# Performance work log

Measured on AMD Instinct MI355X. Metric: run time of the kernel, lower is better.

## Reference

```python
import jax, jax.numpy as jnp
import numpy as np

B, H, S, D = 2, 16, 2048, 64  # batch, heads, seq (q_len=k_len), head dim (d_k=d_v)


def setup_inputs() -> dict:
    key = jax.random.key(0)
    kq, kk, kv = jax.random.split(key, 3)
    Q = jax.random.normal(kq, (B, H, S, D), dtype=jnp.float32)
    K = jax.random.normal(kk, (B, H, S, D), dtype=jnp.float32)
    V = jax.random.normal(kv, (B, H, S, D), dtype=jnp.float32)
    # causal 0/1 mask [q_len, k_len]; zeros get filled with -inf like masked_fill_
    mask = jnp.tril(jnp.ones((S, S), dtype=jnp.int32))
    return {"Q": Q, "K": K, "V": V, "mask": mask}


def reference(Q, K, V, mask):
    scale = K.shape[-1] ** 0.5
    # [B,H,q,k] = Q @ K^T / sqrt(d_k)
    scores = jnp.einsum("bhqd,bhkd->bhqk", Q, K) / scale
    # mask broadcast over batch/heads; mask==0 -> -inf
    scores = jnp.where(mask == 0, jnp.float32(-jnp.inf), scores)
    attn = jax.nn.softmax(scores, axis=-1)
    return jnp.einsum("bhqk,bhkd->bhqd", attn, V)
```

## Files before the change

### kernel.cpp

```cpp
#include <hip/hip_runtime.h>

#define S_LEN 2048
#define DHEAD 64
#define BK 64
#define NBH 32
#define QSCALE 0.18033688011112042f
#define LTHR 1.125899907e15f
#define LSCL 8.881784197e-16f

typedef float f32x4 __attribute__((ext_vector_type(4)));
typedef __bf16 bf16x8 __attribute__((ext_vector_type(8)));
typedef unsigned short u16x8 __attribute__((ext_vector_type(8)));
typedef unsigned short u16x4 __attribute__((ext_vector_type(4)));
typedef unsigned int   u32x4 __attribute__((ext_vector_type(4)));
typedef unsigned int   u32x2 __attribute__((ext_vector_type(2)));

static __device__ __forceinline__ unsigned short bfr(float f) {
    return __builtin_bit_cast(unsigned short, (__bf16)f);
}
static __device__ __forceinline__ int swz(int row, int cb) {
    return row * 128 + (cb ^ ((row & 7) << 4));
}

#if __has_builtin(__builtin_amdgcn_permlane32_swap) && __has_builtin(__builtin_amdgcn_permlane16_swap)
static __device__ __forceinline__ void plswap32(unsigned& a, unsigned& b) {
    u32x2 r = __builtin_amdgcn_permlane32_swap(a, b, false, false);
    a = r[0]; b = r[1];
}
static __device__ __forceinline__ void plswap16(unsigned& a, unsigned& b) {
    u32x2 r = __builtin_amdgcn_permlane16_swap(a, b, false, false);
    a = r[0]; b = r[1];
}
#else
static __device__ __forceinline__ void plswap32(unsigned& a, unsigned& b) {
    asm("v_permlane32_swap_b32 %0, %1" : "+v"(a), "+v"(b));
}
static __device__ __forceinline__ void plswap16(unsigned& a, unsigned& b) {
    asm("v_permlane16_swap_b32 %0, %1" : "+v"(a), "+v"(b));
}
#endif

__global__ __launch_bounds__(256)
void prep(const float* __restrict__ K, const float* __restrict__ V,
          unsigned short* __restrict__ Kb, unsigned short* __restrict__ Vt, int n4) {
    __shared__ unsigned short t2[64][72];
    if ((int)blockIdx.x < 2048) {
        const int stride = 2048 * 256;
        for (int i = (int)blockIdx.x * 256 + threadIdx.x; i < n4; i += stride) {
            f32x4 v = ((const f32x4*)K)[i];
            u16x4 t;
            t[0] = bfr(v[0]); t[1] = bfr(v[1]); t[2] = bfr(v[2]); t[3] = bfr(v[3]);
            ((u16x4*)Kb)[i] = t;
        }
    } else {
        const int bid = (int)blockIdx.x - 2048;
        const int bh = bid >> 5;
        const int st = bid & 31;
        const int t  = threadIdx.x;
        {
            const int sl = t >> 2, d0 = (t & 3) * 16;
            const float* src = V + ((size_t)bh * S_LEN + st * 64 + sl) * DHEAD + d0;
#pragma unroll
            for (int j = 0; j < 4; ++j) {
                f32x4 v = *(const f32x4*)(src + j * 4);
#pragma unroll
                for (int e = 0; e < 4; ++e) t2[sl][d0 + j * 4 + e] = bfr(v[e]);
            }
        }
        __syncthreads();
        const int d = t >> 2, sc = (t & 3) * 16;
        u16x8 a, b;
#pragma unroll
        for (int r = 0; r < 8; ++r) { a[r] = t2[sc + r][d]; b[r] = t2[sc + 8 + r][d]; }
        unsigned short* dst = Vt + ((size_t)bh * DHEAD + d) * S_LEN + st * 64 + sc;
        *(u16x8*)dst = a;
        *(u16x8*)(dst + 8) = b;
    }
}

__global__ __launch_bounds__(256, 3)
void attn_pipe(const float* __restrict__ Qg,
               const unsigned short* __restrict__ Kb,
               const unsigned short* __restrict__ Vt,
               float* __restrict__ Og) {
    __shared__ __align__(16) unsigned short sK[2][BK * DHEAD];
    __shared__ __align__(16) unsigned short sV[2][DHEAD * BK];

    const int tid  = threadIdx.x;
    const int lane = tid & 63;
    const int w    = tid >> 6;
    const int idx = (int)blockIdx.x >> 5;
    const int bh  = (int)blockIdx.x & (NBH - 1);
    const int jj  = idx & 7, k4 = idx >> 3;
    const int blk_q = (k4 == 0) ? 31 - jj : (k4 == 1) ? jj
                    : (k4 == 2) ? 16 + jj : 15 - jj;
    const int q0 = blk_q * 64;
    const size_t base = (size_t)bh * (S_LEN * DHEAD);

    const int c = lane & 15;
    const int h = lane >> 4;

    const int srow = w * 8 + (lane >> 3);
    const int ch8  = ((lane & 7) ^ (lane >> 3)) * 8;
    const unsigned short* pK = Kb + base + (size_t)srow * DHEAD + ch8;
    const unsigned short* pV = Vt + base + (size_t)srow * S_LEN + ch8;

    auto issue = [&](int buf, int kt) {
        unsigned short* dK = &sK[buf][w * 512];
        unsigned short* dV = &sV[buf][w * 512];
        const unsigned short* gk = pK + (size_t)kt * 4096;
        const unsigned short* gv = pV + kt * 64;
#pragma unroll
        for (int i = 0; i < 2; ++i) {
            __builtin_amdgcn_global_load_lds(
                (const __attribute__((address_space(1))) unsigned int*)(gk + i * 2048),
                (__attribute__((address_space(3))) unsigned int*)(dK + i * 2048),
                16, 0, 0);
            __builtin_amdgcn_global_load_lds(
                (const __attribute__((address_space(1))) unsigned int*)(gv + (size_t)i * 32 * S_LEN),
                (__attribute__((address_space(3))) unsigned int*)(dV + i * 2048),
                16, 0, 0);
        }
    };

    bf16x8 qf[2];
    {
        const int qrow = q0 + w * 16 + c;
        const float* qp = Qg + base + (size_t)qrow * DHEAD + h * 8;
#pragma unroll
        for (int kk = 0; kk < 2; ++kk) {
            f32x4 a = *(const f32x4*)(qp + kk * 32);
            f32x4 b = *(const f32x4*)(qp + kk * 32 + 4);
            u16x8 t;
#pragma unroll
            for (int j = 0; j < 4; ++j) {
                t[j]     = bfr(a[j] * QSCALE);
                t[4 + j] = bfr(b[j] * QSCALE);
            }
            qf[kk] = __builtin_bit_cast(bf16x8, t);
        }
    }

    bf16x8 onesf;
    {
        u16x8 t;
#pragma unroll
        for (int j = 0; j < 8; ++j) t[j] = 0x3F80;
        onesf = __builtin_bit_cast(bf16x8, t);
    }

    int offAB[4][2];
#pragma unroll
    for (int n = 0; n < 4; ++n)
#pragma unroll
        for (int kk = 0; kk < 2; ++kk)
            offAB[n][kk] = swz(n * 16 + c, (kk * 32 + h * 8) * 2);

    f32x4 o[4];
#pragma unroll
    for (int dn = 0; dn < 4; ++dn) o[dn] = (f32x4){0.f, 0.f, 0.f, 0.f};
    f32x4 l4 = (f32x4){0.f, 0.f, 0.f, 0.f};
    float m_run = 0.f;
    const int qg = q0 + w * 16 + c;

    issue(0, 0);
    __syncthreads();
    if (blk_q >= 1) issue(1, 1);

    f32x4 st[4];
    {
        const char* sKc = (const char*)&sK[0][0];
#pragma unroll
        for (int n = 0; n < 4; ++n) {
            f32x4 acc = (f32x4){0.f, 0.f, 0.f, 0.f};
#pragma unroll
            for (int kk = 0; kk < 2; ++kk) {
                u16x8 kf = *(const u16x8*)(sKc + offAB[n][kk]);
                acc = __builtin_amdgcn_mfma_f32_16x16x32_bf16(
                        __builtin_bit_cast(bf16x8, kf), qf[kk], acc, 0, 0, 0);
            }
            st[n] = acc;
        }
    }
    bf16x8 vf[4][2];
    {
        const char* sVc = (const char*)&sV[0][0];
#pragma unroll
        for (int dn = 0; dn < 4; ++dn)
#pragma unroll
            for (int kk = 0; kk < 2; ++kk)
                vf[dn][kk] = __builtin_bit_cast(bf16x8,
                                *(const u16x8*)(sVc + offAB[dn][kk]));
    }

    for (int i = 0; i <= blk_q; ++i) {
        f32x4 st2[4];
        if (i < blk_q) {
            __syncthreads();
            if (i + 2 <= blk_q) issue(i & 1, i + 2);

            const char* sKc = (const char*)&sK[(i + 1) & 1][0];
            const float mb = -m_run;
#pragma unroll
            for (int n = 0; n < 4; ++n) {
                f32x4 acc = (f32x4){mb, mb, mb, mb};
#pragma unroll
                for (int kk = 0; kk < 2; ++kk) {
                    u16x8 kf = *(const u16x8*)(sKc + offAB[n][kk]);
                    acc = __builtin_amdgcn_mfma_f32_16x16x32_bf16(
                            __builtin_bit_cast(bf16x8, kf), qf[kk], acc, 0, 0, 0);
                }
                st2[n] = acc;
            }
        }

        if (i == blk_q) {
#pragma unroll
            for (int n = 0; n < 4; ++n)
#pragma unroll
                for (int r = 0; r < 4; ++r)
                    if (i * BK + n * 16 + 4 * h + r > qg) st[n][r] = -INFINITY;
        }

#pragma unroll
        for (int n = 0; n < 4; ++n)
#pragma unroll
            for (int r = 0; r < 4; ++r)
                st[n][r] = exp2f(st[n][r]);

        unsigned pd[4][2];
#pragma unroll
        for (int n = 0; n < 4; ++n) {
            pd[n][0] = (unsigned)bfr(st[n][0]) | ((unsigned)bfr(st[n][1]) << 16);
            pd[n][1] = (unsigned)bfr(st[n][2]) | ((unsigned)bfr(st[n][3]) << 16);
        }
        bf16x8 pb[2];
#pragma unroll
        for (int kk = 0; kk < 2; ++kk) {
            u32x4 fr;
#pragma unroll
            for (int X = 0; X < 2; ++X) {
                unsigned u = pd[2 * kk][X], v = pd[2 * kk + 1][X];
                plswap32(u, v);
                plswap16(u, v);
                fr[X]     = u;
                fr[2 + X] = v;
            }
            pb[kk] = __builtin_bit_cast(bf16x8, fr);
        }

        __builtin_amdgcn_s_setprio(1);
#pragma unroll
        for (int kk = 0; kk < 2; ++kk) {
            l4 = __builtin_amdgcn_mfma_f32_16x16x32_bf16(onesf, pb[kk], l4, 0, 0, 0);
#pragma unroll
            for (int dn = 0; dn < 4; ++dn)
                o[dn] = __builtin_amdgcn_mfma_f32_16x16x32_bf16(
                          vf[dn][kk], pb[kk], o[dn], 0, 0, 0);
        }
        __builtin_amdgcn_s_setprio(0);

        if (i < blk_q) {
            const char* sVc = (const char*)&sV[(i + 1) & 1][0];
#pragma unroll
            for (int dn = 0; dn < 4; ++dn)
#pragma unroll
                for (int kk = 0; kk < 2; ++kk)
                    vf[dn][kk] = __builtin_bit_cast(bf16x8,
                                    *(const u16x8*)(sVc + offAB[dn][kk]));
        }

        if (__builtin_expect(l4[0] > LTHR, 0)) {
            m_run += 50.0f;
            l4 *= LSCL;
#pragma unroll
            for (int dn = 0; dn < 4; ++dn) o[dn] *= LSCL;
            if (i < blk_q) {
#pragma unroll
                for (int n = 0; n < 4; ++n)
#pragma unroll
                    for (int r = 0; r < 4; ++r) st2[n][r] -= 50.0f;
            }
        }

        if (i < blk_q) {
#pragma unroll
            for (int n = 0; n < 4; ++n) st[n] = st2[n];
        }
    }

    const float inv = 1.0f / l4[0];
    float* op = Og + base + (size_t)qg * DHEAD + h * 4;
#pragma unroll
    for (int dn = 0; dn < 4; ++dn) {
        f32x4 t = o[dn] * inv;
        *(f32x4*)(op + dn * 16) = t;
    }
}

__global__ __launch_bounds__(256)
void attn_fb(const float* __restrict__ Qg, const float* __restrict__ K32,
             const float* __restrict__ V32, float* __restrict__ Og) {
    __shared__ __align__(16) unsigned short sK[2][BK * DHEAD];
    __shared__ __align__(16) unsigned short sV[2][DHEAD * BK];
    __shared__ __align__(16) unsigned short sP[4][16 * BK];

    const int tid  = threadIdx.x;
    const int lane = tid & 63;
    const int w    = tid >> 6;
    const int blk_q = 31 - ((int)blockIdx.x >> 5);
    const int bh    = (int)blockIdx.x & (NBH - 1);
    const int q0    = blk_q * 64;
    const size_t base = (size_t)bh * (S_LEN * DHEAD);

    const int col = lane & 15;
    const int hi  = lane >> 4;
    const int vkb = (tid >> 4) * 4;
    const int vdb = (tid & 15) * 4;
    const int fkr = tid >> 2;
    const int fkc = (tid & 3) * 16;

    f32x4 kr32[4], vr32[4];
    auto stage_issue = [&](int kt) {
        const float* kp = K32 + base + (size_t)(kt * BK + fkr) * DHEAD + fkc;
#pragma unroll
        for (int j = 0; j < 4; ++j) kr32[j] = *(const f32x4*)(kp + j * 4);
        const float* vp = V32 + base + (size_t)(kt * BK + vkb) * DHEAD + vdb;
#pragma unroll
        for (int j = 0; j < 4; ++j) vr32[j] = *(const f32x4*)(vp + j * DHEAD);
    };
    auto stage_write = [&](int buf) {
        char* sKb_ = (char*)&sK[buf][0];
        char* sVb_ = (char*)&sV[buf][0];
        u16x8 p0, p1;
#pragma unroll
        for (int j = 0; j < 4; ++j) {
            p0[j] = bfr(kr32[0][j]); p0[4 + j] = bfr(kr32[1][j]);
            p1[j] = bfr(kr32[2][j]); p1[4 + j] = bfr(kr32[3][j]);
        }
        *(u16x8*)(sKb_ + swz(fkr, fkc * 2))      = p0;
        *(u16x8*)(sKb_ + swz(fkr, fkc * 2 + 16)) = p1;
#pragma unroll
        for (int dd = 0; dd < 4; ++dd) {
            u16x4 t;
#pragma unroll
            for (int j = 0; j < 4; ++j) t[j] = bfr(vr32[j][dd]);
            *(u16x4*)(sVb_ + swz(vdb + dd, vkb * 2)) = t;
        }
    };

    bf16x8 qf[2];
    {
        const int qrow = q0 + w * 16 + col;
        const float* qp = Qg + base + (size_t)qrow * DHEAD + hi * 8;
#pragma unroll
        for (int kk = 0; kk < 2; ++kk) {
            f32x4 a = *(const f32x4*)(qp + kk * 32);
            f32x4 b = *(const f32x4*)(qp + kk * 32 + 4);
            u16x8 t;
#pragma unroll
            for (int j = 0; j < 4; ++j) {
                t[j]     = bfr(a[j] * QSCALE);
                t[4 + j] = bfr(b[j] * QSCALE);
            }
            qf[kk] = __builtin_bit_cast(bf16x8, t);
        }
    }

    int offAB[4][2];
#pragma unroll
    for (int n = 0; n < 4; ++n)
#pragma unroll
        for (int kk = 0; kk < 2; ++kk)
            offAB[n][kk] = swz(n * 16 + col, (kk * 32 + hi * 8) * 2);
    char* sPw = (char*)&sP[w][0];
    int offPS[4], offPL[2];
#pragma unroll
    for (int n = 0; n < 4; ++n)
        offPS[n] = col * 128 + ((n * 32 + hi * 8) ^ ((col & 7) << 4));
#pragma unroll
    for (int kk = 0; kk < 2; ++kk)
        offPL[kk] = col * 128 + ((kk * 64 + hi * 16) ^ ((col & 7) << 4));

    f32x4 o[4];
#pragma unroll
    for (int dn = 0; dn < 4; ++dn) o[dn] = (f32x4){0.f, 0.f, 0.f, 0.f};
    float m_run = -INFINITY, l_run = 0.f;

    stage_issue(0);
    stage_write(0);
    __syncthreads();

    int cur = 0;
    for (int kt = 0; kt <= blk_q; ++kt) {
        const char* sKc = (const char*)&sK[cur][0];
        const char* sVc = (const char*)&sV[cur][0];
        if (kt < blk_q) stage_issue(kt + 1);

        f32x4 st[4];
#pragma unroll
        for (int n = 0; n < 4; ++n) {
            f32x4 acc = (f32x4){0.f, 0.f, 0.f, 0.f};
#pragma unroll
            for (int kk = 0; kk < 2; ++kk) {
                u16x8 kf = *(const u16x8*)(sKc + offAB[n][kk]);
                acc = __builtin_amdgcn_mfma_f32_16x16x32_bf16(
                        __builtin_bit_cast(bf16x8, kf), qf[kk], acc, 0, 0, 0);
            }
            st[n] = acc;
        }
        if (kt == blk_q) {
            const int qg = q0 + w * 16 + col;
#pragma unroll
            for (int n = 0; n < 4; ++n)
#pragma unroll
                for (int r = 0; r < 4; ++r)
                    if (kt * BK + n * 16 + hi * 4 + r > qg) st[n][r] = -INFINITY;
        }
        float mx = fmaxf(fmaxf(st[0][0], st[0][1]), fmaxf(st[0][2], st[0][3]));
#pragma unroll
        for (int n = 1; n < 4; ++n)
            mx = fmaxf(mx, fmaxf(fmaxf(st[n][0], st[n][1]), fmaxf(st[n][2], st[n][3])));
        mx = fmaxf(mx, __shfl_xor(mx, 16));
        mx = fmaxf(mx, __shfl_xor(mx, 32));
        if (!__all(mx <= m_run + 8.0f)) {
            const float mn = fmaxf(m_run, mx);
            const float al = exp2f(m_run - mn);
            m_run = mn;
            l_run *= al;
#pragma unroll
            for (int dn = 0; dn < 4; ++dn) o[dn] *= al;
        }
        float sum = 0.f;
#pragma unroll
        for (int n = 0; n < 4; ++n)
#pragma unroll
            for (int r = 0; r < 4; ++r) {
                float p = exp2f(st[n][r] - m_run);
                st[n][r] = p;
                sum += p;
            }
        sum += __shfl_xor(sum, 16);
        sum += __shfl_xor(sum, 32);
        l_run += sum;
#pragma unroll
        for (int n = 0; n < 4; ++n) {
            u16x4 t;
#pragma unroll
            for (int r = 0; r < 4; ++r) t[r] = bfr(st[n][r]);
            *(u16x4*)(sPw + offPS[n]) = t;
        }
        bf16x8 pb[2];
#pragma unroll
        for (int kk = 0; kk < 2; ++kk)
            pb[kk] = __builtin_bit_cast(bf16x8, *(const u16x8*)(sPw + offPL[kk]));
#pragma unroll
        for (int dn = 0; dn < 4; ++dn)
#pragma unroll
            for (int kk = 0; kk < 2; ++kk) {
                u16x8 vfr = *(const u16x8*)(sVc + offAB[dn][kk]);
                o[dn] = __builtin_amdgcn_mfma_f32_16x16x32_bf16(
                          __builtin_bit_cast(bf16x8, vfr), pb[kk], o[dn], 0, 0, 0);
            }
        if (kt < blk_q) stage_write(cur ^ 1);
        __syncthreads();
        cur ^= 1;
    }

    const float inv = 1.0f / l_run;
    const int qg = q0 + w * 16 + col;
    float* op = Og + base + (size_t)qg * DHEAD + hi * 4;
#pragma unroll
    for (int dn = 0; dn < 4; ++dn) {
        f32x4 t = o[dn] * inv;
        *(f32x4*)(op + dn * 16) = t;
    }
}

extern "C" void kernel_launch(void* const* d_in, const int* in_sizes, int n_in,
                              void* d_out, int out_size, void* d_ws, size_t ws_size,
                              hipStream_t stream) {
    const float* Q = (const float*)d_in[0];
    const float* K = (const float*)d_in[1];
    const float* V = (const float*)d_in[2];
    float* O = (float*)d_out;

    const size_t nelem   = (size_t)NBH * S_LEN * DHEAD;
    const size_t kvBytes = 2 * nelem * sizeof(unsigned short);

    if (ws_size >= kvBytes) {
        unsigned short* Kb = (unsigned short*)d_ws;
        unsigned short* Vt = Kb + nelem;
        prep<<<3072, 256, 0, stream>>>(K, V, Kb, Vt, (int)(nelem / 4));
        attn_pipe<<<dim3(32 * NBH), 256, 0, stream>>>(Q, Kb, Vt, O);
    } else {
        attn_fb<<<dim3(32 * NBH), 256, 0, stream>>>(Q, K, V, O);
    }
}
```

Baseline: 54.05 us.

## Replace LDS double-buffered K/V pipeline with direct global-to-register loads

The attention kernel no longer stages K and V tiles through shared memory with async global-to-LDS loads and barriers. Each wave now loads its K and V fragments straight from global memory into registers, relying on L2/L1 for reuse across the four waves of a block. It also drops the software pipelining that computed the next tile's scores early, and replaces the load-balanced query-block ordering with a simple descending order. This removes barrier and LDS traffic but multiplies global/L1 reads by the wave count and exposes load latency without explicit prefetch.

```diff
diff --git a/kernel.cpp b/kernel.cpp
--- a/kernel.cpp
+++ b/kernel.cpp
@@ -79,54 +79,25 @@
 }
 
 __global__ __launch_bounds__(256, 3)
-void attn_pipe(const float* __restrict__ Qg,
-               const unsigned short* __restrict__ Kb,
-               const unsigned short* __restrict__ Vt,
-               float* __restrict__ Og) {
-    __shared__ __align__(16) unsigned short sK[2][BK * DHEAD];
-    __shared__ __align__(16) unsigned short sV[2][DHEAD * BK];
-
+void attn_nb(const float* __restrict__ Qg,
+             const unsigned short* __restrict__ Kb,
+             const unsigned short* __restrict__ Vt,
+             float* __restrict__ Og) {
     const int tid  = threadIdx.x;
     const int lane = tid & 63;
     const int w    = tid >> 6;
-    const int idx = (int)blockIdx.x >> 5;
-    const int bh  = (int)blockIdx.x & (NBH - 1);
-    const int jj  = idx & 7, k4 = idx >> 3;
-    const int blk_q = (k4 == 0) ? 31 - jj : (k4 == 1) ? jj
-                    : (k4 == 2) ? 16 + jj : 15 - jj;
-    const int q0 = blk_q * 64;
+    const int bh   = (int)blockIdx.x & (NBH - 1);
+    const int qb   = 31 - ((int)blockIdx.x >> 5);
+    const int q0   = qb * 64;
     const size_t base = (size_t)bh * (S_LEN * DHEAD);
 
     const int c = lane & 15;
     const int h = lane >> 4;
-
-    const int srow = w * 8 + (lane >> 3);
-    const int ch8  = ((lane & 7) ^ (lane >> 3)) * 8;
-    const unsigned short* pK = Kb + base + (size_t)srow * DHEAD + ch8;
-    const unsigned short* pV = Vt + base + (size_t)srow * S_LEN + ch8;
-
-    auto issue = [&](int buf, int kt) {
-        unsigned short* dK = &sK[buf][w * 512];
-        unsigned short* dV = &sV[buf][w * 512];
-        const unsigned short* gk = pK + (size_t)kt * 4096;
-        const unsigned short* gv = pV + kt * 64;
-#pragma unroll
-        for (int i = 0; i < 2; ++i) {
-            __builtin_amdgcn_global_load_lds(
-                (const __attribute__((address_space(1))) unsigned int*)(gk + i * 2048),
-                (__attribute__((address_space(3))) unsigned int*)(dK + i * 2048),
-                16, 0, 0);
-            __builtin_amdgcn_global_load_lds(
-                (const __attribute__((address_space(1))) unsigned int*)(gv + (size_t)i * 32 * S_LEN),
-                (__attribute__((address_space(3))) unsigned int*)(dV + i * 2048),
-                16, 0, 0);
-        }
-    };
+    const int qg = q0 + w * 16 + c;
 
     bf16x8 qf[2];
     {
-        const int qrow = q0 + w * 16 + c;
-        const float* qp = Qg + base + (size_t)qrow * DHEAD + h * 8;
+        const float* qp = Qg + base + (size_t)qg * DHEAD + h * 8;
 #pragma unroll
         for (int kk = 0; kk < 2; ++kk) {
             f32x4 a = *(const f32x4*)(qp + kk * 32);
@@ -149,77 +120,53 @@
         onesf = __builtin_bit_cast(bf16x8, t);
     }
 
-    int offAB[4][2];
-#pragma unroll
-    for (int n = 0; n < 4; ++n)
-#pragma unroll
-        for (int kk = 0; kk < 2; ++kk)
-            offAB[n][kk] = swz(n * 16 + c, (kk * 32 + h * 8) * 2);
+    const unsigned short* pK = Kb + base + (size_t)c * 64 + h * 8;
+    const unsigned short* pV = Vt + base + (size_t)c * S_LEN + h * 8;
 
     f32x4 o[4];
 #pragma unroll
     for (int dn = 0; dn < 4; ++dn) o[dn] = (f32x4){0.f, 0.f, 0.f, 0.f};
     f32x4 l4 = (f32x4){0.f, 0.f, 0.f, 0.f};
     float m_run = 0.f;
-    const int qg = q0 + w * 16 + c;
-
-    issue(0, 0);
-    __syncthreads();
-    if (blk_q >= 1) issue(1, 1);
-
-    f32x4 st[4];
-    {
-        const char* sKc = (const char*)&sK[0][0];
+
+    for (int kt = 0; kt <= qb; ++kt) {
+        const unsigned short* pKt = pK + kt * (BK * DHEAD);
+        const unsigned short* pVt = pV + kt * BK;
+
+        u16x8 kr[4][2];
+#pragma unroll
+        for (int n = 0; n < 4; ++n)
+#pragma unroll
+            for (int kk = 0; kk < 2; ++kk)
+                kr[n][kk] = *(const u16x8*)(pKt + n * (16 * DHEAD) + kk * 32);
+
+        const float mb = -m_run;
+        f32x4 st[4];
+        __builtin_amdgcn_s_setprio(1);
 #pragma unroll
         for (int n = 0; n < 4; ++n) {
-            f32x4 acc = (f32x4){0.f, 0.f, 0.f, 0.f};
-#pragma unroll
-            for (int kk = 0; kk < 2; ++kk) {
-                u16x8 kf = *(const u16x8*)(sKc + offAB[n][kk]);
+            f32x4 acc = (f32x4){mb, mb, mb, mb};
+#pragma unroll
+            for (int kk = 0; kk < 2; ++kk)
                 acc = __builtin_amdgcn_mfma_f32_16x16x32_bf16(
-                        __builtin_bit_cast(bf16x8, kf), qf[kk], acc, 0, 0, 0);
-            }
+                        __builtin_bit_cast(bf16x8, kr[n][kk]), qf[kk], acc, 0, 0, 0);
             st[n] = acc;
         }
-    }
-    bf16x8 vf[4][2];
-    {
-        const char* sVc = (const char*)&sV[0][0];
+        __builtin_amdgcn_s_setprio(0);
+
+        u16x8 vr[4][2];
 #pragma unroll
         for (int dn = 0; dn < 4; ++dn)
 #pragma unroll
             for (int kk = 0; kk < 2; ++kk)
-                vf[dn][kk] = __builtin_bit_cast(bf16x8,
-                                *(const u16x8*)(sVc + offAB[dn][kk]));
-    }
-
-    for (int i = 0; i <= blk_q; ++i) {
-        f32x4 st2[4];
-        if (i < blk_q) {
-            __syncthreads();
-            if (i + 2 <= blk_q) issue(i & 1, i + 2);
-
-            const char* sKc = (const char*)&sK[(i + 1) & 1][0];
-            const float mb = -m_run;
-#pragma unroll
-            for (int n = 0; n < 4; ++n) {
-                f32x4 acc = (f32x4){mb, mb, mb, mb};
-#pragma unroll
-                for (int kk = 0; kk < 2; ++kk) {
-                    u16x8 kf = *(const u16x8*)(sKc + offAB[n][kk]);
-                    acc = __builtin_amdgcn_mfma_f32_16x16x32_bf16(
-                            __builtin_bit_cast(bf16x8, kf), qf[kk], acc, 0, 0, 0);
-                }
-                st2[n] = acc;
-            }
-        }
-
-        if (i == blk_q) {
+                vr[dn][kk] = *(const u16x8*)(pVt + dn * (16 * S_LEN) + kk * 32);
+
+        if (kt == qb) {
 #pragma unroll
             for (int n = 0; n < 4; ++n)
 #pragma unroll
                 for (int r = 0; r < 4; ++r)
-                    if (i * BK + n * 16 + 4 * h + r > qg) st[n][r] = -INFINITY;
+                    if (kt * BK + n * 16 + 4 * h + r > qg) st[n][r] = -INFINITY;
         }
 
 #pragma unroll
@@ -256,36 +203,15 @@
 #pragma unroll
             for (int dn = 0; dn < 4; ++dn)
                 o[dn] = __builtin_amdgcn_mfma_f32_16x16x32_bf16(
-                          vf[dn][kk], pb[kk], o[dn], 0, 0, 0);
+                          __builtin_bit_cast(bf16x8, vr[dn][kk]), pb[kk], o[dn], 0, 0, 0);
         }
         __builtin_amdgcn_s_setprio(0);
-
-        if (i < blk_q) {
-            const char* sVc = (const char*)&sV[(i + 1) & 1][0];
-#pragma unroll
-            for (int dn = 0; dn < 4; ++dn)
-#pragma unroll
-                for (int kk = 0; kk < 2; ++kk)
-                    vf[dn][kk] = __builtin_bit_cast(bf16x8,
-                                    *(const u16x8*)(sVc + offAB[dn][kk]));
-        }
 
         if (__builtin_expect(l4[0] > LTHR, 0)) {
             m_run += 50.0f;
             l4 *= LSCL;
 #pragma unroll
             for (int dn = 0; dn < 4; ++dn) o[dn] *= LSCL;
-            if (i < blk_q) {
-#pragma unroll
-                for (int n = 0; n < 4; ++n)
-#pragma unroll
-                    for (int r = 0; r < 4; ++r) st2[n][r] -= 50.0f;
-            }
-        }
-
-        if (i < blk_q) {
-#pragma unroll
-            for (int n = 0; n < 4; ++n) st[n] = st2[n];
         }
     }
 
@@ -492,7 +418,7 @@
         unsigned short* Kb = (unsigned short*)d_ws;
         unsigned short* Vt = Kb + nelem;
         prep<<<3072, 256, 0, stream>>>(K, V, Kb, Vt, (int)(nelem / 4));
-        attn_pipe<<<dim3(32 * NBH), 256, 0, stream>>>(Q, Kb, Vt, O);
+        attn_nb<<<dim3(32 * NBH), 256, 0, stream>>>(Q, Kb, Vt, O);
     } else {
         attn_fb<<<dim3(32 * NBH), 256, 0, stream>>>(Q, K, V, O);
     }
```

After: 157.9 us. 2.92x slower.

## Split key dimension across warps with LDS reduction instead of per-warp query rows

Applied to the files above, without the earlier changes.

The attention kernel now gives each warp a 16-key slice of every 64-key tile across all 64 query rows, rather than 16 query rows across all keys. P stays in the MFMA output layout and feeds 16x16x16 MFMAs directly, which removes the permlane swaps and the running-max rescale check. Partial O and row sums from the four warps are combined through LDS at the end. The cost is more accumulator registers (occupancy hint lowered from 3 to 2), an end-of-kernel reduction, and no max subtraction, so exp2 overflow safety depends on the input score range.

```diff
diff --git a/kernel.cpp b/kernel.cpp
--- a/kernel.cpp
+++ b/kernel.cpp
@@ -5,15 +5,13 @@
 #define BK 64
 #define NBH 32
 #define QSCALE 0.18033688011112042f
-#define LTHR 1.125899907e15f
-#define LSCL 8.881784197e-16f
 
 typedef float f32x4 __attribute__((ext_vector_type(4)));
 typedef __bf16 bf16x8 __attribute__((ext_vector_type(8)));
+typedef __bf16 bf16x4 __attribute__((ext_vector_type(4)));
+typedef short  s16x4  __attribute__((ext_vector_type(4)));
 typedef unsigned short u16x8 __attribute__((ext_vector_type(8)));
 typedef unsigned short u16x4 __attribute__((ext_vector_type(4)));
-typedef unsigned int   u32x4 __attribute__((ext_vector_type(4)));
-typedef unsigned int   u32x2 __attribute__((ext_vector_type(2)));
 
 static __device__ __forceinline__ unsigned short bfr(float f) {
     return __builtin_bit_cast(unsigned short, (__bf16)f);
@@ -22,23 +20,19 @@
     return row * 128 + (cb ^ ((row & 7) << 4));
 }
 
-#if __has_builtin(__builtin_amdgcn_permlane32_swap) && __has_builtin(__builtin_amdgcn_permlane16_swap)
-static __device__ __forceinline__ void plswap32(unsigned& a, unsigned& b) {
-    u32x2 r = __builtin_amdgcn_permlane32_swap(a, b, false, false);
-    a = r[0]; b = r[1];
-}
-static __device__ __forceinline__ void plswap16(unsigned& a, unsigned& b) {
-    u32x2 r = __builtin_amdgcn_permlane16_swap(a, b, false, false);
-    a = r[0]; b = r[1];
-}
+static __device__ __forceinline__ f32x4 mfma16(bf16x4 a, bf16x4 b, f32x4 c) {
+#if __has_builtin(__builtin_amdgcn_mfma_f32_16x16x16_bf16)
+    return __builtin_amdgcn_mfma_f32_16x16x16_bf16(a, b, c, 0, 0, 0);
+#elif __has_builtin(__builtin_amdgcn_mfma_f32_16x16x16bf16_1k)
+    return __builtin_amdgcn_mfma_f32_16x16x16bf16_1k(
+        __builtin_bit_cast(s16x4, a), __builtin_bit_cast(s16x4, b), c, 0, 0, 0);
 #else
-static __device__ __forceinline__ void plswap32(unsigned& a, unsigned& b) {
-    asm("v_permlane32_swap_b32 %0, %1" : "+v"(a), "+v"(b));
-}
-static __device__ __forceinline__ void plswap16(unsigned& a, unsigned& b) {
-    asm("v_permlane16_swap_b32 %0, %1" : "+v"(a), "+v"(b));
-}
+    f32x4 d;
+    asm volatile("v_mfma_f32_16x16x16_bf16 %0, %1, %2, %3"
+                 : "=&v"(d) : "v"(a), "v"(b), "v"(c));
+    return d;
 #endif
+}
 
 __global__ __launch_bounds__(256)
 void prep(const float* __restrict__ K, const float* __restrict__ V,
@@ -78,13 +72,12 @@
     }
 }
 
-__global__ __launch_bounds__(256, 3)
-void attn_pipe(const float* __restrict__ Qg,
-               const unsigned short* __restrict__ Kb,
-               const unsigned short* __restrict__ Vt,
-               float* __restrict__ Og) {
-    __shared__ __align__(16) unsigned short sK[2][BK * DHEAD];
-    __shared__ __align__(16) unsigned short sV[2][DHEAD * BK];
+__global__ __launch_bounds__(256, 2)
+void attn_ks(const float* __restrict__ Qg,
+             const unsigned short* __restrict__ Kb,
+             const unsigned short* __restrict__ Vt,
+             float* __restrict__ Og) {
+    __shared__ __align__(16) char smem[35328];
 
     const int tid  = threadIdx.x;
     const int lane = tid & 63;
@@ -92,9 +85,9 @@
     const int idx = (int)blockIdx.x >> 5;
     const int bh  = (int)blockIdx.x & (NBH - 1);
     const int jj  = idx & 7, k4 = idx >> 3;
-    const int blk_q = (k4 == 0) ? 31 - jj : (k4 == 1) ? jj
-                    : (k4 == 2) ? 16 + jj : 15 - jj;
-    const int q0 = blk_q * 64;
+    const int qb  = (k4 == 0) ? 31 - jj : (k4 == 1) ? jj
+                  : (k4 == 2) ? 16 + jj : 15 - jj;
+    const int q0  = qb * 64;
     const size_t base = (size_t)bh * (S_LEN * DHEAD);
 
     const int c = lane & 15;
@@ -106,8 +99,8 @@
     const unsigned short* pV = Vt + base + (size_t)srow * S_LEN + ch8;
 
     auto issue = [&](int buf, int kt) {
-        unsigned short* dK = &sK[buf][w * 512];
-        unsigned short* dV = &sV[buf][w * 512];
+        unsigned short* dK = (unsigned short*)(smem + buf * 16384) + w * 512;
+        unsigned short* dV = (unsigned short*)(smem + buf * 16384 + 8192) + w * 512;
         const unsigned short* gk = pK + (size_t)kt * 4096;
         const unsigned short* gv = pV + kt * 64;
 #pragma unroll
@@ -123,9 +116,10 @@
         }
     };
 
-    bf16x8 qf[2];
-    {
-        const int qrow = q0 + w * 16 + c;
+    bf16x8 qf[4][2];
+#pragma unroll
+    for (int qg = 0; qg < 4; ++qg) {
+        const int qrow = q0 + qg * 16 + c;
         const float* qp = Qg + base + (size_t)qrow * DHEAD + h * 8;
 #pragma unroll
         for (int kk = 0; kk < 2; ++kk) {
@@ -137,164 +131,176 @@
                 t[j]     = bfr(a[j] * QSCALE);
                 t[4 + j] = bfr(b[j] * QSCALE);
             }
-            qf[kk] = __builtin_bit_cast(bf16x8, t);
-        }
-    }
-
-    bf16x8 onesf;
+            qf[qg][kk] = __builtin_bit_cast(bf16x8, t);
+        }
+    }
+
+    bf16x4 ones4;
     {
-        u16x8 t;
-#pragma unroll
-        for (int j = 0; j < 8; ++j) t[j] = 0x3F80;
-        onesf = __builtin_bit_cast(bf16x8, t);
-    }
-
-    int offAB[4][2];
-#pragma unroll
-    for (int n = 0; n < 4; ++n)
-#pragma unroll
-        for (int kk = 0; kk < 2; ++kk)
-            offAB[n][kk] = swz(n * 16 + c, (kk * 32 + h * 8) * 2);
-
-    f32x4 o[4];
-#pragma unroll
-    for (int dn = 0; dn < 4; ++dn) o[dn] = (f32x4){0.f, 0.f, 0.f, 0.f};
-    f32x4 l4 = (f32x4){0.f, 0.f, 0.f, 0.f};
-    float m_run = 0.f;
-    const int qg = q0 + w * 16 + c;
+        u16x4 t;
+#pragma unroll
+        for (int j = 0; j < 4; ++j) t[j] = 0x3F80;
+        ones4 = __builtin_bit_cast(bf16x4, t);
+    }
+
+    int offKA[2], offV[4];
+#pragma unroll
+    for (int kk = 0; kk < 2; ++kk)
+        offKA[kk] = swz(16 * w + c, (kk * 32 + h * 8) * 2);
+#pragma unroll
+    for (int dg = 0; dg < 4; ++dg)
+        offV[dg] = swz(dg * 16 + c, (16 * w + 4 * h) * 2);
+
+    int thr[4];
+#pragma unroll
+    for (int qg = 0; qg < 4; ++qg)
+        thr[qg] = qg * 16 + c - 16 * w - 4 * h;
+
+    f32x4 o[4][4];
+#pragma unroll
+    for (int dg = 0; dg < 4; ++dg)
+#pragma unroll
+        for (int qg = 0; qg < 4; ++qg) o[dg][qg] = (f32x4){0.f, 0.f, 0.f, 0.f};
+    f32x4 l4[4];
+#pragma unroll
+    for (int qg = 0; qg < 4; ++qg) l4[qg] = (f32x4){0.f, 0.f, 0.f, 0.f};
 
     issue(0, 0);
     __syncthreads();
-    if (blk_q >= 1) issue(1, 1);
+    if (qb >= 1) issue(1, 1);
 
     f32x4 st[4];
     {
-        const char* sKc = (const char*)&sK[0][0];
-#pragma unroll
-        for (int n = 0; n < 4; ++n) {
+        const char* Kc = smem;
+        bf16x8 kr0 = __builtin_bit_cast(bf16x8, *(const u16x8*)(Kc + offKA[0]));
+        bf16x8 kr1 = __builtin_bit_cast(bf16x8, *(const u16x8*)(Kc + offKA[1]));
+#pragma unroll
+        for (int qg = 0; qg < 4; ++qg) {
             f32x4 acc = (f32x4){0.f, 0.f, 0.f, 0.f};
-#pragma unroll
-            for (int kk = 0; kk < 2; ++kk) {
-                u16x8 kf = *(const u16x8*)(sKc + offAB[n][kk]);
-                acc = __builtin_amdgcn_mfma_f32_16x16x32_bf16(
-                        __builtin_bit_cast(bf16x8, kf), qf[kk], acc, 0, 0, 0);
-            }
-            st[n] = acc;
-        }
-    }
-    bf16x8 vf[4][2];
+            acc = __builtin_amdgcn_mfma_f32_16x16x32_bf16(kr0, qf[qg][0], acc, 0, 0, 0);
+            acc = __builtin_amdgcn_mfma_f32_16x16x32_bf16(kr1, qf[qg][1], acc, 0, 0, 0);
+            st[qg] = acc;
+        }
+        if (qb == 0) {
+#pragma unroll
+            for (int qg = 0; qg < 4; ++qg)
+#pragma unroll
+                for (int r = 0; r < 4; ++r)
+                    if (r > thr[qg]) st[qg][r] = -INFINITY;
+        }
+    }
+
+    for (int i = 0; i <= qb; ++i) {
+        const char* Vc = smem + (i & 1) * 16384 + 8192;
+        bf16x4 vf[4];
+#pragma unroll
+        for (int dg = 0; dg < 4; ++dg)
+            vf[dg] = __builtin_bit_cast(bf16x4, *(const u16x4*)(Vc + offV[dg]));
+
+        f32x4 st2[4];
+        if (i < qb) {
+            __syncthreads();
+            if (i + 2 <= qb) issue(i & 1, i + 2);
+
+            const char* Kc = smem + ((i + 1) & 1) * 16384;
+            bf16x8 kr0 = __builtin_bit_cast(bf16x8, *(const u16x8*)(Kc + offKA[0]));
+            bf16x8 kr1 = __builtin_bit_cast(bf16x8, *(const u16x8*)(Kc + offKA[1]));
+            __builtin_amdgcn_s_setprio(1);
+#pragma unroll
+            for (int qg = 0; qg < 4; ++qg) {
+                f32x4 acc = (f32x4){0.f, 0.f, 0.f, 0.f};
+                acc = __builtin_amdgcn_mfma_f32_16x16x32_bf16(kr0, qf[qg][0], acc, 0, 0, 0);
+                acc = __builtin_amdgcn_mfma_f32_16x16x32_bf16(kr1, qf[qg][1], acc, 0, 0, 0);
+                st2[qg] = acc;
+            }
+            __builtin_amdgcn_s_setprio(0);
+            if (i + 1 == qb) {
+#pragma unroll
+                for (int qg = 0; qg < 4; ++qg)
+#pragma unroll
+                    for (int r = 0; r < 4; ++r)
+                        if (r > thr[qg]) st2[qg][r] = -INFINITY;
+            }
+        }
+
+        bf16x4 pb[4];
+#pragma unroll
+        for (int qg = 0; qg < 4; ++qg) {
+            u16x4 t;
+#pragma unroll
+            for (int r = 0; r < 4; ++r)
+                t[r] = bfr(exp2f(st[qg][r]));
+            pb[qg] = __builtin_bit_cast(bf16x4, t);
+        }
+
+        __builtin_amdgcn_s_setprio(1);
+#pragma unroll
+        for (int qg = 0; qg < 4; ++qg)
+            l4[qg] = mfma16(ones4, pb[qg], l4[qg]);
+#pragma unroll
+        for (int dg = 0; dg < 4; ++dg)
+#pragma unroll
+            for (int qg = 0; qg < 4; ++qg)
+                o[dg][qg] = mfma16(vf[dg], pb[qg], o[dg][qg]);
+        __builtin_amdgcn_s_setprio(0);
+
+        if (i < qb) {
+#pragma unroll
+            for (int qg = 0; qg < 4; ++qg) st[qg] = st2[qg];
+        }
+    }
+
+    float* OA = (float*)smem;
+    float* OB = (float*)(smem + 17408);
+    float* lA = (float*)(smem + 34816);
+    float* lB = (float*)(smem + 35072);
+
+    __syncthreads();
     {
-        const char* sVc = (const char*)&sV[0][0];
-#pragma unroll
-        for (int dn = 0; dn < 4; ++dn)
-#pragma unroll
-            for (int kk = 0; kk < 2; ++kk)
-                vf[dn][kk] = __builtin_bit_cast(bf16x8,
-                                *(const u16x8*)(sVc + offAB[dn][kk]));
-    }
-
-    for (int i = 0; i <= blk_q; ++i) {
-        f32x4 st2[4];
-        if (i < blk_q) {
-            __syncthreads();
-            if (i + 2 <= blk_q) issue(i & 1, i + 2);
-
-            const char* sKc = (const char*)&sK[(i + 1) & 1][0];
-            const float mb = -m_run;
-#pragma unroll
-            for (int n = 0; n < 4; ++n) {
-                f32x4 acc = (f32x4){mb, mb, mb, mb};
-#pragma unroll
-                for (int kk = 0; kk < 2; ++kk) {
-                    u16x8 kf = *(const u16x8*)(sKc + offAB[n][kk]);
-                    acc = __builtin_amdgcn_mfma_f32_16x16x32_bf16(
-                            __builtin_bit_cast(bf16x8, kf), qf[kk], acc, 0, 0, 0);
+        float* Or = (w & 1) ? OB : OA;
+        float* lr = (w & 1) ? lB : lA;
+        if (w < 2) {
+#pragma unroll
+            for (int dg = 0; dg < 4; ++dg)
+#pragma unroll
+                for (int qg = 0; qg < 4; ++qg)
+                    *(f32x4*)&Or[(qg * 16 + c) * 68 + dg * 16 + 4 * h] = o[dg][qg];
+            if (h == 0) {
+#pragma unroll
+                for (int qg = 0; qg < 4; ++qg)
+                    lr[qg * 16 + c] = l4[qg][0];
+            }
+        }
+        __syncthreads();
+        if (w >= 2) {
+#pragma unroll
+            for (int dg = 0; dg < 4; ++dg)
+#pragma unroll
+                for (int qg = 0; qg < 4; ++qg) {
+                    float* p = &Or[(qg * 16 + c) * 68 + dg * 16 + 4 * h];
+                    f32x4 t = *(f32x4*)p + o[dg][qg];
+                    *(f32x4*)p = t;
                 }
-                st2[n] = acc;
-            }
-        }
-
-        if (i == blk_q) {
-#pragma unroll
-            for (int n = 0; n < 4; ++n)
-#pragma unroll
-                for (int r = 0; r < 4; ++r)
-                    if (i * BK + n * 16 + 4 * h + r > qg) st[n][r] = -INFINITY;
-        }
-
-#pragma unroll
-        for (int n = 0; n < 4; ++n)
-#pragma unroll
-            for (int r = 0; r < 4; ++r)
-                st[n][r] = exp2f(st[n][r]);
-
-        unsigned pd[4][2];
-#pragma unroll
-        for (int n = 0; n < 4; ++n) {
-            pd[n][0] = (unsigned)bfr(st[n][0]) | ((unsigned)bfr(st[n][1]) << 16);
-            pd[n][1] = (unsigned)bfr(st[n][2]) | ((unsigned)bfr(st[n][3]) << 16);
-        }
-        bf16x8 pb[2];
-#pragma unroll
-        for (int kk = 0; kk < 2; ++kk) {
-            u32x4 fr;
-#pragma unroll
-            for (int X = 0; X < 2; ++X) {
-                unsigned u = pd[2 * kk][X], v = pd[2 * kk + 1][X];
-                plswap32(u, v);
-                plswap16(u, v);
-                fr[X]     = u;
-                fr[2 + X] = v;
-            }
-            pb[kk] = __builtin_bit_cast(bf16x8, fr);
-        }
-
-        __builtin_amdgcn_s_setprio(1);
-#pragma unroll
-        for (int kk = 0; kk < 2; ++kk) {
-            l4 = __builtin_amdgcn_mfma_f32_16x16x32_bf16(onesf, pb[kk], l4, 0, 0, 0);
-#pragma unroll
-            for (int dn = 0; dn < 4; ++dn)
-                o[dn] = __builtin_amdgcn_mfma_f32_16x16x32_bf16(
-                          vf[dn][kk], pb[kk], o[dn], 0, 0, 0);
-        }
-        __builtin_amdgcn_s_setprio(0);
-
-        if (i < blk_q) {
-            const char* sVc = (const char*)&sV[(i + 1) & 1][0];
-#pragma unroll
-            for (int dn = 0; dn < 4; ++dn)
-#pragma unroll
-                for (int kk = 0; kk < 2; ++kk)
-                    vf[dn][kk] = __builtin_bit_cast(bf16x8,
-                                    *(const u16x8*)(sVc + offAB[dn][kk]));
-        }
-
-        if (__builtin_expect(l4[0] > LTHR, 0)) {
-            m_run += 50.0f;
-            l4 *= LSCL;
-#pragma unroll
-            for (int dn = 0; dn < 4; ++dn) o[dn] *= LSCL;
-            if (i < blk_q) {
-#pragma unroll
-                for (int n = 0; n < 4; ++n)
-#pragma unroll
-                    for (int r = 0; r < 4; ++r) st2[n][r] -= 50.0f;
-            }
-        }
-
-        if (i < blk_q) {
-#pragma unroll
-            for (int n = 0; n < 4; ++n) st[n] = st2[n];
-        }
-    }
-
-    const float inv = 1.0f / l4[0];
-    float* op = Og + base + (size_t)qg * DHEAD + h * 4;
-#pragma unroll
-    for (int dn = 0; dn < 4; ++dn) {
-        f32x4 t = o[dn] * inv;
-        *(f32x4*)(op + dn * 16) = t;
+            if (h == 0) {
+#pragma unroll
+                for (int qg = 0; qg < 4; ++qg)
+                    lr[qg * 16 + c] += l4[qg][0];
+            }
+        }
+        __syncthreads();
+    }
+
+    {
+        const int q = 16 * w + c;
+        const float inv = 1.0f / (lA[q] + lB[q]);
+        float* op = Og + base + (size_t)(q0 + q) * DHEAD;
+#pragma unroll
+        for (int g = 0; g < 4; ++g) {
+            f32x4 a = *(f32x4*)&OA[q * 68 + g * 16 + 4 * h];
+            f32x4 b = *(f32x4*)&OB[q * 68 + g * 16 + 4 * h];
+            f32x4 t = (a + b) * inv;
+            *(f32x4*)(op + g * 16 + 4 * h) = t;
+        }
     }
 }
 
@@ -492,7 +498,7 @@
         unsigned short* Kb = (unsigned short*)d_ws;
         unsigned short* Vt = Kb + nelem;
         prep<<<3072, 256, 0, stream>>>(K, V, Kb, Vt, (int)(nelem / 4));
-        attn_pipe<<<dim3(32 * NBH), 256, 0, stream>>>(Q, Kb, Vt, O);
+        attn_ks<<<dim3(32 * NBH), 256, 0, stream>>>(Q, Kb, Vt, O);
     } else {
         attn_fb<<<dim3(32 * NBH), 256, 0, stream>>>(Q, K, V, O);
     }
```

Result: slower. 60.86 us (+12.6%).
